# Kernel tuning notes

Measured on AMD Instinct MI355X. Metric: run time of the kernel, lower is better.

## Reference

```python
import jax, jax.numpy as jnp
import numpy as np

TT_SHAPES = [16, 16, 16, 16, 16, 16]
TT_RANKS = [1, 64, 64, 64, 64, 64, 1]
OUT_FEATURES = 4096  # 16*16*16
IN_FEATURES = 4096   # 16*16*16
N_TOKENS = 8192


def setup_inputs() -> dict:
    key = jax.random.key(0)
    ks = jax.random.split(key, len(TT_SHAPES) + 2)
    inp = {}
    for i in range(len(TT_SHAPES)):
        shape = (TT_RANKS[i], TT_SHAPES[i], TT_RANKS[i + 1])
        # xavier-uniform-like init
        fan = TT_RANKS[i] * TT_SHAPES[i] + TT_SHAPES[i] * TT_RANKS[i + 1]
        bound = float(np.sqrt(6.0 / fan))
        inp[f"core{i}"] = jax.random.uniform(ks[i], shape, jnp.float32, -bound, bound)
    inp["x"] = jax.random.normal(ks[-2], (N_TOKENS, IN_FEATURES), dtype=jnp.float32)
    b_bound = 1.0 / np.sqrt(IN_FEATURES)
    inp["b"] = jax.random.uniform(ks[-1], (OUT_FEATURES,), jnp.float32, -b_bound, b_bound)
    return inp


def _recover_weight(cores):
    # chain of reshape+matmul contractions, exactly as TTLinearR._recover_weight
    w = cores[0]
    for i in range(1, len(cores)):
        w = w.reshape(-1, TT_RANKS[i]) @ cores[i].reshape(TT_RANKS[i], -1)
    return w.reshape(OUT_FEATURES, IN_FEATURES)


def reference(x, core0, core1, core2, core3, core4, core5, b):
    w = _recover_weight([core0, core1, core2, core3, core4, core5])
    # F.linear(x, w, b) == x @ w.T + b
    return x @ w.T + b
```

## Files before the change

kernel.cpp:

```cpp
#include <hip/hip_runtime.h>


#define TOK 8192
#define DIN 4096
#define DOUT 4096
#define RNK 64

typedef __bf16 bf16x8 __attribute__((ext_vector_type(8)));
typedef float f32x4 __attribute__((ext_vector_type(4)));

__device__ __forceinline__ unsigned short f2bf(float f) {
  unsigned int u = __float_as_uint(f);
  u += 0x7FFFu + ((u >> 16) & 1u);
  return (unsigned short)(u >> 16);
}

__global__ void mm64_kernel(const float* __restrict__ A, const float* __restrict__ B,
                            float* __restrict__ C, int N) {
  int idx = blockIdx.x * 256 + threadIdx.x;
  int m = idx / N;
  int n = idx - m * N;
  const float* a = A + m * 64;
  float acc = 0.f;
#pragma unroll
  for (int k = 0; k < 64; ++k) acc += a[k] * B[k * N + n];
  C[idx] = acc;
}

#define G1_SX 136
__global__ __launch_bounds__(256, 2)
void gemm1_mfma(const float* __restrict__ x, const float* __restrict__ Bmat,
                float* __restrict__ t) {
  __shared__ unsigned short xs[64 * G1_SX];
  __shared__ unsigned short bs[64 * G1_SX];
  const int tid = threadIdx.x;
  const int m0 = blockIdx.y * 64;
  const int lane = tid & 63, wv = tid >> 6;
  const int r = lane & 15, q = lane >> 4;

  f32x4 acc[4];
#pragma unroll
  for (int j = 0; j < 4; ++j) acc[j] = (f32x4){0.f, 0.f, 0.f, 0.f};

  for (int s = 0; s < 4; ++s) {
    const int kbase = blockIdx.z * 512 + s * 128;
#pragma unroll
    for (int j = 0; j < 8; ++j) {
      int f = j * 256 + tid;
      int row = f >> 5, c4 = f & 31;
      float4 vx = *(const float4*)&x[(size_t)(m0 + row) * DIN + kbase + c4 * 4];
      ushort4 hx = {f2bf(vx.x), f2bf(vx.y), f2bf(vx.z), f2bf(vx.w)};
      *(ushort4*)&xs[row * G1_SX + c4 * 4] = hx;
      float4 vb = *(const float4*)&Bmat[(size_t)row * DIN + kbase + c4 * 4];
      ushort4 hb = {f2bf(vb.x), f2bf(vb.y), f2bf(vb.z), f2bf(vb.w)};
      *(ushort4*)&bs[row * G1_SX + c4 * 4] = hb;
    }
    __syncthreads();
#pragma unroll
    for (int s32 = 0; s32 < 4; ++s32) {
      bf16x8 a = *(const bf16x8*)&xs[(wv * 16 + r) * G1_SX + s32 * 32 + q * 8];
#pragma unroll
      for (int j = 0; j < 4; ++j) {
        bf16x8 b = *(const bf16x8*)&bs[(j * 16 + r) * G1_SX + s32 * 32 + q * 8];
        acc[j] = __builtin_amdgcn_mfma_f32_16x16x32_bf16(a, b, acc[j], 0, 0, 0);
      }
    }
    __syncthreads();
  }
#pragma unroll
  for (int j = 0; j < 4; ++j)
#pragma unroll
    for (int i = 0; i < 4; ++i)
      atomicAdd(&t[(size_t)(m0 + wv * 16 + q * 4 + i) * RNK + j * 16 + r], acc[j][i]);
}

#define G2_S 72
__global__ __launch_bounds__(256, 2)
void gemm2_mfma(const float* __restrict__ t, const float* __restrict__ Amat,
                const float* __restrict__ bias, float* __restrict__ out) {
  __shared__ unsigned short ts[128 * G2_S];
  __shared__ unsigned short as_[128 * G2_S];
  const int tid = threadIdx.x;
  const int m0 = blockIdx.y * 128, n0 = blockIdx.x * 128;
  const int lane = tid & 63, wv = tid >> 6;
  const int r = lane & 15, q = lane >> 4;

#pragma unroll
  for (int j = 0; j < 8; ++j) {
    int f = j * 256 + tid;
    int row = f >> 4, c4 = f & 15;
    float4 vt = *(const float4*)&t[(size_t)(m0 + row) * RNK + c4 * 4];
    ushort4 ht = {f2bf(vt.x), f2bf(vt.y), f2bf(vt.z), f2bf(vt.w)};
    *(ushort4*)&ts[row * G2_S + c4 * 4] = ht;
    float4 va = *(const float4*)&Amat[(size_t)(n0 + row) * RNK + c4 * 4];
    ushort4 ha = {f2bf(va.x), f2bf(va.y), f2bf(va.z), f2bf(va.w)};
    *(ushort4*)&as_[row * G2_S + c4 * 4] = ha;
  }
  __syncthreads();

  const int mw = (wv >> 1) * 64, nw = (wv & 1) * 64;
  f32x4 acc[4][4];
#pragma unroll
  for (int i = 0; i < 4; ++i)
#pragma unroll
    for (int j = 0; j < 4; ++j) acc[i][j] = (f32x4){0.f, 0.f, 0.f, 0.f};

#pragma unroll
  for (int s32 = 0; s32 < 2; ++s32) {
    bf16x8 a[4], b[4];
#pragma unroll
    for (int i = 0; i < 4; ++i)
      a[i] = *(const bf16x8*)&ts[(mw + i * 16 + r) * G2_S + s32 * 32 + q * 8];
#pragma unroll
    for (int j = 0; j < 4; ++j)
      b[j] = *(const bf16x8*)&as_[(nw + j * 16 + r) * G2_S + s32 * 32 + q * 8];
#pragma unroll
    for (int i = 0; i < 4; ++i)
#pragma unroll
      for (int j = 0; j < 4; ++j)
        acc[i][j] = __builtin_amdgcn_mfma_f32_16x16x32_bf16(a[i], b[j], acc[i][j], 0, 0, 0);
  }

  float bb[4];
#pragma unroll
  for (int j = 0; j < 4; ++j) bb[j] = bias[n0 + nw + j * 16 + r];

#pragma unroll
  for (int i = 0; i < 4; ++i)
#pragma unroll
    for (int reg = 0; reg < 4; ++reg) {
      size_t rowg = (size_t)(m0 + mw + i * 16 + q * 4 + reg) * DOUT;
#pragma unroll
      for (int j = 0; j < 4; ++j)
        out[rowg + n0 + nw + j * 16 + r] = acc[i][j][reg] + bb[j];
    }
}

extern "C" void kernel_launch(void* const* d_in, const int* in_sizes, int n_in,
                              void* d_out, int out_size, void* d_ws, size_t ws_size,
                              hipStream_t stream) {
  const float* c0 = (const float*)d_in[0];
  const float* c1 = (const float*)d_in[1];
  const float* c2 = (const float*)d_in[2];
  const float* c3 = (const float*)d_in[3];
  const float* c4 = (const float*)d_in[4];
  const float* c5 = (const float*)d_in[5];
  const float* x  = (const float*)d_in[6];
  const float* bias = (const float*)d_in[7];
  float* out = (float*)d_out;

  char* ws = (char*)d_ws;
  float* t    = (float*)(ws);
  float* Amat = (float*)(ws + (2u << 20));
  float* Bmat = (float*)(ws + (3u << 20));
  float* S1   = (float*)(ws + (4u << 20));
  float* S3   = (float*)(ws + (4u << 20) + (1u << 17));

  hipMemsetAsync(t, 0, (size_t)TOK * RNK * sizeof(float), stream);

  mm64_kernel<<<(16 * 1024) / 256, 256, 0, stream>>>(c0, c1, S1, 1024);
  mm64_kernel<<<(256 * 1024) / 256, 256, 0, stream>>>(S1, c2, Amat, 1024);
  mm64_kernel<<<(1024 * 16) / 256, 256, 0, stream>>>(c4, c5, S3, 16);
  mm64_kernel<<<(1024 * 256) / 256, 256, 0, stream>>>(c3, S3, Bmat, 256);

  gemm1_mfma<<<dim3(1, TOK / 64, 8), 256, 0, stream>>>(x, Bmat, t);

  gemm2_mfma<<<dim3(DOUT / 128, TOK / 128), 256, 0, stream>>>(t, Amat, bias, out);
}
```

Before: 288.7 us.

## Replace atomic split-K with partial buffers plus reduce, precompute bf16 factors

The factor-matrix kernels now write bf16 directly, so the two GEMMs load pre-converted bf16 tiles with 16-byte copies instead of converting fp32 every time. The split-K atomicAdd accumulation into t is replaced by per-split partial buffers, which lets the memset go away. A new reduce kernel sums the eight partials and emits bf16 t for the second GEMM. In exchange it adds an extra kernel launch and about 16 MB of partial-buffer traffic, and drops the min-blocks occupancy hint.

```diff
diff --git a/kernel.cpp b/kernel.cpp
--- a/kernel.cpp
+++ b/kernel.cpp
@@ -5,6 +5,7 @@
 #define DIN 4096
 #define DOUT 4096
 #define RNK 64
+#define KSPLIT 8
 
 typedef __bf16 bf16x8 __attribute__((ext_vector_type(8)));
 typedef float f32x4 __attribute__((ext_vector_type(4)));
@@ -27,23 +28,36 @@
   C[idx] = acc;
 }
 
+__global__ void mm64_bf16_kernel(const float* __restrict__ A, const float* __restrict__ B,
+                                 unsigned short* __restrict__ C, int N) {
+  int idx = blockIdx.x * 256 + threadIdx.x;
+  int m = idx / N;
+  int n = idx - m * N;
+  const float* a = A + m * 64;
+  float acc = 0.f;
+#pragma unroll
+  for (int k = 0; k < 64; ++k) acc += a[k] * B[k * N + n];
+  C[idx] = f2bf(acc);
+}
+
 #define G1_SX 136
-__global__ __launch_bounds__(256, 2)
-void gemm1_mfma(const float* __restrict__ x, const float* __restrict__ Bmat,
-                float* __restrict__ t) {
+__global__ __launch_bounds__(256)
+void gemm1_mfma(const float* __restrict__ x, const unsigned short* __restrict__ Bbf,
+                float* __restrict__ t_part) {
   __shared__ unsigned short xs[64 * G1_SX];
   __shared__ unsigned short bs[64 * G1_SX];
   const int tid = threadIdx.x;
   const int m0 = blockIdx.y * 64;
   const int lane = tid & 63, wv = tid >> 6;
   const int r = lane & 15, q = lane >> 4;
+  const int z = blockIdx.z;
 
   f32x4 acc[4];
 #pragma unroll
   for (int j = 0; j < 4; ++j) acc[j] = (f32x4){0.f, 0.f, 0.f, 0.f};
 
   for (int s = 0; s < 4; ++s) {
-    const int kbase = blockIdx.z * 512 + s * 128;
+    const int kbase = z * (DIN / KSPLIT) + s * 128;
 #pragma unroll
     for (int j = 0; j < 8; ++j) {
       int f = j * 256 + tid;
@@ -51,9 +65,13 @@
       float4 vx = *(const float4*)&x[(size_t)(m0 + row) * DIN + kbase + c4 * 4];
       ushort4 hx = {f2bf(vx.x), f2bf(vx.y), f2bf(vx.z), f2bf(vx.w)};
       *(ushort4*)&xs[row * G1_SX + c4 * 4] = hx;
-      float4 vb = *(const float4*)&Bmat[(size_t)row * DIN + kbase + c4 * 4];
-      ushort4 hb = {f2bf(vb.x), f2bf(vb.y), f2bf(vb.z), f2bf(vb.w)};
-      *(ushort4*)&bs[row * G1_SX + c4 * 4] = hb;
+    }
+#pragma unroll
+    for (int j = 0; j < 4; ++j) {
+      int f = j * 256 + tid;
+      int row = f >> 4, c = f & 15;
+      *(uint4*)&bs[row * G1_SX + c * 8] =
+          *(const uint4*)&Bbf[(size_t)row * DIN + kbase + c * 8];
     }
     __syncthreads();
 #pragma unroll
@@ -67,16 +85,29 @@
     }
     __syncthreads();
   }
+  float* tp = t_part + ((size_t)z * TOK + m0 + wv * 16 + q * 4) * RNK + r;
 #pragma unroll
   for (int j = 0; j < 4; ++j)
 #pragma unroll
     for (int i = 0; i < 4; ++i)
-      atomicAdd(&t[(size_t)(m0 + wv * 16 + q * 4 + i) * RNK + j * 16 + r], acc[j][i]);
+      tp[(size_t)i * RNK + j * 16] = acc[j][i];
+}
+
+__global__ void reduce_t(const float* __restrict__ t_part, unsigned short* __restrict__ tbf) {
+  int i4 = (blockIdx.x * 256 + threadIdx.x) * 4;
+  float4 s = *(const float4*)&t_part[i4];
+#pragma unroll
+  for (int z = 1; z < KSPLIT; ++z) {
+    float4 p = *(const float4*)&t_part[(size_t)z * TOK * RNK + i4];
+    s.x += p.x; s.y += p.y; s.z += p.z; s.w += p.w;
+  }
+  ushort4 h = {f2bf(s.x), f2bf(s.y), f2bf(s.z), f2bf(s.w)};
+  *(ushort4*)&tbf[i4] = h;
 }
 
 #define G2_S 72
-__global__ __launch_bounds__(256, 2)
-void gemm2_mfma(const float* __restrict__ t, const float* __restrict__ Amat,
+__global__ __launch_bounds__(256)
+void gemm2_mfma(const unsigned short* __restrict__ tbf, const unsigned short* __restrict__ Abf,
                 const float* __restrict__ bias, float* __restrict__ out) {
   __shared__ unsigned short ts[128 * G2_S];
   __shared__ unsigned short as_[128 * G2_S];
@@ -86,15 +117,13 @@
   const int r = lane & 15, q = lane >> 4;
 
 #pragma unroll
-  for (int j = 0; j < 8; ++j) {
+  for (int j = 0; j < 4; ++j) {
     int f = j * 256 + tid;
-    int row = f >> 4, c4 = f & 15;
-    float4 vt = *(const float4*)&t[(size_t)(m0 + row) * RNK + c4 * 4];
-    ushort4 ht = {f2bf(vt.x), f2bf(vt.y), f2bf(vt.z), f2bf(vt.w)};
-    *(ushort4*)&ts[row * G2_S + c4 * 4] = ht;
-    float4 va = *(const float4*)&Amat[(size_t)(n0 + row) * RNK + c4 * 4];
-    ushort4 ha = {f2bf(va.x), f2bf(va.y), f2bf(va.z), f2bf(va.w)};
-    *(ushort4*)&as_[row * G2_S + c4 * 4] = ha;
+    int row = f >> 3, c = f & 7;
+    *(uint4*)&ts[row * G2_S + c * 8] =
+        *(const uint4*)&tbf[(size_t)(m0 + row) * RNK + c * 8];
+    *(uint4*)&as_[row * G2_S + c * 8] =
+        *(const uint4*)&Abf[(size_t)(n0 + row) * RNK + c * 8];
   }
   __syncthreads();
 
@@ -150,20 +179,21 @@
   float* out = (float*)d_out;
 
   char* ws = (char*)d_ws;
-  float* t    = (float*)(ws);
-  float* Amat = (float*)(ws + (2u << 20));
-  float* Bmat = (float*)(ws + (3u << 20));
-  float* S1   = (float*)(ws + (4u << 20));
-  float* S3   = (float*)(ws + (4u << 20) + (1u << 17));
-
-  hipMemsetAsync(t, 0, (size_t)TOK * RNK * sizeof(float), stream);
+  float*          t_part = (float*)(ws);
+  unsigned short* tbf    = (unsigned short*)(ws + (16u << 20));
+  unsigned short* Abf    = (unsigned short*)(ws + (17u << 20));
+  unsigned short* Bbf    = (unsigned short*)(ws + (17u << 20) + (1u << 19));
+  float*          S1     = (float*)(ws + (18u << 20));
+  float*          S3     = (float*)(ws + (18u << 20) + (1u << 16));
 
   mm64_kernel<<<(16 * 1024) / 256, 256, 0, stream>>>(c0, c1, S1, 1024);
-  mm64_kernel<<<(256 * 1024) / 256, 256, 0, stream>>>(S1, c2, Amat, 1024);
+  mm64_bf16_kernel<<<(256 * 1024) / 256, 256, 0, stream>>>(S1, c2, Abf, 1024);
   mm64_kernel<<<(1024 * 16) / 256, 256, 0, stream>>>(c4, c5, S3, 16);
-  mm64_kernel<<<(1024 * 256) / 256, 256, 0, stream>>>(c3, S3, Bmat, 256);
+  mm64_bf16_kernel<<<(1024 * 256) / 256, 256, 0, stream>>>(c3, S3, Bbf, 256);
 
-  gemm1_mfma<<<dim3(1, TOK / 64, 8), 256, 0, stream>>>(x, Bmat, t);
+  gemm1_mfma<<<dim3(1, TOK / 64, KSPLIT), 256, 0, stream>>>(x, Bbf, t_part);
 
-  gemm2_mfma<<<dim3(DOUT / 128, TOK / 128), 256, 0, stream>>>(t, Amat, bias, out);
+  reduce_t<<<(TOK * RNK / 4) / 256, 256, 0, stream>>>(t_part, tbf);
+
+  gemm2_mfma<<<dim3(DOUT / 128, TOK / 128), 256, 0, stream>>>(tbf, Abf, bias, out);
 }
```

New measurement: 281.6 us. 1.03x faster.
